# Kernel tuning notes

Hardware: AMD Instinct MI355X
Metric: run time of the kernel (lower is better)

Reference implementation:

```python
import jax, jax.numpy as jnp
import numpy as np

B, N, DIM = 8, 1024, 1024
H, DH = 16, 64           # heads, dim_head; inner_dim = H*DH = 1024
SCALE = DH ** -0.5


def setup_inputs() -> dict:
    key = jax.random.key(0)
    k_x, k_qkv, k_out, k_b = jax.random.split(key, 4)
    inner = H * DH
    x = jax.random.normal(k_x, (B, N, DIM), dtype=jnp.float32)
    # nn.Linear(dim, inner*3, bias=False): y = x @ W_qkv
    W_qkv = jax.random.normal(k_qkv, (DIM, 3 * inner), dtype=jnp.float32) * (DIM ** -0.5)
    # nn.Linear(inner, dim) with bias (project_out is True since heads!=1)
    W_out = jax.random.normal(k_out, (inner, DIM), dtype=jnp.float32) * (inner ** -0.5)
    b_out = jax.random.normal(k_b, (DIM,), dtype=jnp.float32) * 0.01
    return {"x": x, "W_qkv": W_qkv, "W_out": W_out, "b_out": b_out}


def reference(x, W_qkv, W_out, b_out):
    # 'trans' branch of Attention.forward (dropout p=0 -> identity)
    qkv = x @ W_qkv                                   # [b, n, 3*inner]
    q, k, v = jnp.split(qkv, 3, axis=-1)              # each [b, n, inner]
    def to_heads(t):
        b, n, _ = t.shape
        return t.reshape(b, n, H, DH).transpose(0, 2, 1, 3)  # [b, h, n, d]
    q, k, v = to_heads(q), to_heads(k), to_heads(v)
    dots = jnp.einsum('bhid,bhjd->bhij', q, k) * SCALE  # [b, h, n, n]
    attn = jax.nn.softmax(dots, axis=-1)
    out = jnp.einsum('bhij,bhjd->bhid', attn, v)        # [b, h, n, d]
    # original sets attn = out (b h n d) before merging heads
    attn_ret = out
    out_m = out.transpose(0, 2, 1, 3).reshape(B, N, H * DH)  # [b, n, inner]
    proj = out_m @ W_out + b_out                        # [b, n, dim]
    return (proj, attn_ret)
```

## Files before the change

### kernel.cpp

```cpp
#include <hip/hip_runtime.h>
#include <hip/hip_bf16.h>
#include <math.h>

typedef __bf16 bf16_t;
typedef __bf16 bf16x8 __attribute__((ext_vector_type(8)));
typedef __bf16 bf16x4 __attribute__((ext_vector_type(4)));
typedef float f32x4 __attribute__((ext_vector_type(4)));

#define MFMA16(a, b, c) __builtin_amdgcn_mfma_f32_16x16x32_bf16((a), (b), (c), 0, 0, 0)

#define AS3(p) ((__attribute__((address_space(3))) void*)(p))
#define AS1(p) ((const __attribute__((address_space(1))) void*)(p))

#define B_ 8
#define N_ 1024
#define DIM_ 1024
#define H_ 16
#define DH_ 64

#define QSCALE 0.18033688011112042f
#define SM_SHIFT 12.0f

__global__ __launch_bounds__(256) void k_convert(const float* __restrict__ in,
                                                 bf16_t* __restrict__ out) {
    size_t idx = ((size_t)blockIdx.x * 256 + threadIdx.x) * 8;
    f32x4 a = *(const f32x4*)(in + idx);
    f32x4 b = *(const f32x4*)(in + idx + 4);
    bf16x8 o;
    o[0] = (bf16_t)a[0]; o[1] = (bf16_t)a[1]; o[2] = (bf16_t)a[2]; o[3] = (bf16_t)a[3];
    o[4] = (bf16_t)b[0]; o[5] = (bf16_t)b[1]; o[6] = (bf16_t)b[2]; o[7] = (bf16_t)b[3];
    *(bf16x8*)(out + idx) = o;
}

__global__ __launch_bounds__(256) void k_prep_w(const float* __restrict__ Wqkv,
                                                bf16_t* __restrict__ wqkvt,
                                                const float* __restrict__ Wout,
                                                bf16_t* __restrict__ woutt) {
    __shared__ float tile[32][33];
    int bx = blockIdx.x;
    const float* in;
    bf16_t* out;
    int C, cb;
    if (bx < 96) { in = Wqkv; out = wqkvt; C = 3072; cb = bx; }
    else         { in = Wout; out = woutt; C = 1024; cb = bx - 96; }
    const int R = 1024;
    int c0 = cb * 32, r0 = blockIdx.y * 32;
    int tx = threadIdx.x, ty = threadIdx.y;
#pragma unroll
    for (int i = 0; i < 4; ++i)
        tile[ty + 8 * i][tx] = in[(size_t)(r0 + ty + 8 * i) * C + (c0 + tx)];
    __syncthreads();
#pragma unroll
    for (int i = 0; i < 4; ++i)
        out[(size_t)(c0 + ty + 8 * i) * R + (r0 + tx)] = (bf16_t)tile[tx][ty + 8 * i];
}

__global__ __launch_bounds__(256, 2) void k_gemm_qkv(const bf16_t* __restrict__ A,
                                                     const bf16_t* __restrict__ Bt,
                                                     bf16_t* __restrict__ qb,
                                                     bf16_t* __restrict__ kbuf,
                                                     bf16_t* __restrict__ vtb) {
    __shared__ __align__(16) bf16_t As[256 * 64];
    __shared__ __align__(16) bf16_t Bs[128 * 64];
    int tid = threadIdx.x;
    int lane = tid & 63, wave = tid >> 6;
    int quad = lane >> 4, l16 = lane & 15;
    int m0 = blockIdx.y * 256, c0 = blockIdx.x * 128;
    int wm = (wave & 1) * 128, wn = (wave >> 1) * 64;

    const f32x4 vzero = {0.f, 0.f, 0.f, 0.f};
    f32x4 acc[8][4];
#pragma unroll
    for (int i = 0; i < 8; ++i)
#pragma unroll
        for (int j = 0; j < 4; ++j) acc[i][j] = vzero;

    for (int k0 = 0; k0 < 1024; k0 += 64) {
#pragma unroll
        for (int i = 0; i < 8; ++i) {
            int cid = tid + 256 * i;
            int row = cid >> 3;
            int g = (cid & 7) ^ (row & 7);
            __builtin_amdgcn_global_load_lds(
                AS1(A + (size_t)(m0 + row) * 1024 + k0 + g * 8), AS3(As + cid * 8), 16, 0, 0);
        }
#pragma unroll
        for (int i = 0; i < 4; ++i) {
            int cid = tid + 256 * i;
            int row = cid >> 3;
            int g = (cid & 7) ^ (row & 7);
            __builtin_amdgcn_global_load_lds(
                AS1(Bt + (size_t)(c0 + row) * 1024 + k0 + g * 8), AS3(Bs + cid * 8), 16, 0, 0);
        }
        __syncthreads();
#pragma unroll
        for (int c = 0; c < 2; ++c) {
            int s = (4 * c + quad) ^ (l16 & 7);
            bf16x8 bfr[4];
#pragma unroll
            for (int j = 0; j < 4; ++j)
                bfr[j] = *(const bf16x8*)(Bs + (wn + 16 * j + l16) * 64 + s * 8);
#pragma unroll
            for (int i = 0; i < 8; ++i) {
                bf16x8 af = *(const bf16x8*)(As + (wm + 16 * i + l16) * 64 + s * 8);
#pragma unroll
                for (int j = 0; j < 4; ++j)
                    acc[i][j] = MFMA16(af, bfr[j], acc[i][j]);
            }
        }
        __syncthreads();
    }

    int tsel = c0 >> 10;
#pragma unroll
    for (int i = 0; i < 8; ++i) {
#pragma unroll
        for (int r = 0; r < 4; ++r) {
            int m = m0 + wm + 16 * i + quad * 4 + r;
            int b = m >> 10, n = m & 1023;
#pragma unroll
            for (int j = 0; j < 4; ++j) {
                int cc = c0 + wn + 16 * j + l16;
                int ic = cc & 1023;
                int h = ic >> 6, d = ic & 63;
                float val = acc[i][j][r];
                if (tsel == 0)
                    qb[(((size_t)b * H_ + h) * N_ + n) * DH_ + d] = (bf16_t)(val * QSCALE);
                else if (tsel == 1)
                    kbuf[(((size_t)b * H_ + h) * N_ + n) * DH_ + d] = (bf16_t)val;
                else
                    vtb[(((size_t)b * H_ + h) * DH_ + d) * N_ + n] = (bf16_t)val;
            }
        }
    }
}

__global__ __launch_bounds__(256, 2) void k_attn(const bf16_t* __restrict__ q,
                                                 const bf16_t* __restrict__ k,
                                                 const bf16_t* __restrict__ vt,
                                                 float* __restrict__ oattn,
                                                 bf16_t* __restrict__ outm) {
    __shared__ __align__(16) bf16_t Ks[64 * 64];
    __shared__ __align__(16) bf16_t Vs[64 * 64];
    __shared__ __align__(16) bf16_t Ps[4 * 4 * 16 * 72];
    int tid = threadIdx.x;
    int lane = tid & 63, wave = tid >> 6;
    int quad = lane >> 4, l16 = lane & 15;
    int qt = blockIdx.x & 3;
    int bh = blockIdx.x >> 2;
    int b = bh >> 4, h = bh & 15;

    const bf16_t* qp = q + ((size_t)bh * N_ + qt * 256 + wave * 64) * DH_;
    bf16x8 qa[4][2];
#pragma unroll
    for (int g = 0; g < 4; ++g)
#pragma unroll
        for (int c = 0; c < 2; ++c)
            qa[g][c] = *(const bf16x8*)(qp + (size_t)(g * 16 + l16) * DH_ + c * 32 + quad * 8);

    const bf16_t* kp = k + (size_t)bh * N_ * DH_;
    const bf16_t* vp = vt + (size_t)bh * DH_ * N_;
    bf16_t* Pw = Ps + wave * (4 * 16 * 72);

    const f32x4 vzero = {0.f, 0.f, 0.f, 0.f};
    f32x4 o[4][4];
#pragma unroll
    for (int g = 0; g < 4; ++g)
#pragma unroll
        for (int t = 0; t < 4; ++t) o[g][t] = vzero;
    float lsum[4] = {0.f, 0.f, 0.f, 0.f};

    for (int kb = 0; kb < 16; ++kb) {
#pragma unroll
        for (int i = 0; i < 2; ++i) {
            int cid = tid + 256 * i;
            int row = cid >> 3;
            int g = (cid & 7) ^ (row & 7);
            __builtin_amdgcn_global_load_lds(
                AS1(kp + (size_t)(kb * 64 + row) * DH_ + g * 8), AS3(Ks + cid * 8), 16, 0, 0);
            __builtin_amdgcn_global_load_lds(
                AS1(vp + (size_t)row * N_ + kb * 64 + g * 8), AS3(Vs + cid * 8), 16, 0, 0);
        }
        __syncthreads();

        f32x4 st[4][4];
#pragma unroll
        for (int jt = 0; jt < 4; ++jt) {
#pragma unroll
            for (int g = 0; g < 4; ++g) st[g][jt] = vzero;
#pragma unroll
            for (int c = 0; c < 2; ++c) {
                int s = (4 * c + quad) ^ (l16 & 7);
                bf16x8 kf = *(const bf16x8*)(Ks + (16 * jt + l16) * 64 + s * 8);
#pragma unroll
                for (int g = 0; g < 4; ++g)
                    st[g][jt] = MFMA16(kf, qa[g][c], st[g][jt]);
            }
        }

#pragma unroll
        for (int g = 0; g < 4; ++g) {
            float ps = 0.f;
#pragma unroll
            for (int jt = 0; jt < 4; ++jt) {
                bf16x4 pk;
#pragma unroll
                for (int r = 0; r < 4; ++r) {
                    float p = __builtin_amdgcn_exp2f(st[g][jt][r] - SM_SHIFT);
                    ps += p;
                    pk[r] = (bf16_t)p;
                }
                *(bf16x4*)(Pw + g * (16 * 72) + l16 * 72 + jt * 16 + quad * 4) = pk;
            }
            lsum[g] += ps;
        }

        bf16x8 pf[4][2];
#pragma unroll
        for (int g = 0; g < 4; ++g)
#pragma unroll
            for (int c = 0; c < 2; ++c)
                pf[g][c] = *(const bf16x8*)(Pw + g * (16 * 72) + l16 * 72 + c * 32 + quad * 8);
#pragma unroll
        for (int t = 0; t < 4; ++t)
#pragma unroll
            for (int c = 0; c < 2; ++c) {
                int s = (4 * c + quad) ^ (l16 & 7);
                bf16x8 vf = *(const bf16x8*)(Vs + (16 * t + l16) * 64 + s * 8);
#pragma unroll
                for (int g = 0; g < 4; ++g)
                    o[g][t] = MFMA16(vf, pf[g][c], o[g][t]);
            }
        __syncthreads();
    }

#pragma unroll
    for (int g = 0; g < 4; ++g) {
        lsum[g] += __shfl_xor(lsum[g], 16);
        lsum[g] += __shfl_xor(lsum[g], 32);
    }

    float* Ot = (float*)Ps + wave * 16 * 68;
#pragma unroll
    for (int g = 0; g < 4; ++g) {
        float inv = 1.f / lsum[g];
#pragma unroll
        for (int t = 0; t < 4; ++t) {
            f32x4 v4;
#pragma unroll
            for (int r = 0; r < 4; ++r) v4[r] = o[g][t][r] * inv;
            *(f32x4*)(Ot + l16 * 68 + t * 16 + quad * 4) = v4;
        }
        int row = lane >> 2, cl = lane & 3;
        int n = qt * 256 + wave * 64 + g * 16 + row;
        const float* orow = Ot + row * 68 + cl * 16;
        float* gout = oattn + ((size_t)bh * N_ + n) * DH_ + cl * 16;
        bf16_t* gm = outm + ((size_t)b * N_ + n) * DIM_ + h * DH_ + cl * 16;
#pragma unroll
        for (int s = 0; s < 4; ++s) {
            f32x4 v = *(const f32x4*)(orow + s * 4);
            *(f32x4*)(gout + s * 4) = v;
            bf16x4 vb;
#pragma unroll
            for (int r = 0; r < 4; ++r) vb[r] = (bf16_t)v[r];
            *(bf16x4*)(gm + s * 4) = vb;
        }
    }
}

__global__ __launch_bounds__(256) void k_gemm_proj(const bf16_t* __restrict__ A,
                                                   const bf16_t* __restrict__ Bt,
                                                   const float* __restrict__ bias,
                                                   float* __restrict__ out) {
    __shared__ __align__(16) bf16_t As[128 * 64];
    __shared__ __align__(16) bf16_t Bs[128 * 64];
    int tid = threadIdx.x;
    int lane = tid & 63, wave = tid >> 6;
    int quad = lane >> 4, l16 = lane & 15;
    int m0 = blockIdx.y * 128, c0 = blockIdx.x * 128;
    int wm = (wave & 1) * 64, wn = (wave >> 1) * 64;

    const f32x4 vzero = {0.f, 0.f, 0.f, 0.f};
    f32x4 acc[4][4];
#pragma unroll
    for (int i = 0; i < 4; ++i)
#pragma unroll
        for (int j = 0; j < 4; ++j) acc[i][j] = vzero;

    for (int k0 = 0; k0 < 1024; k0 += 64) {
#pragma unroll
        for (int i = 0; i < 4; ++i) {
            int cid = tid + 256 * i;
            int row = cid >> 3;
            int g = (cid & 7) ^ (row & 7);
            __builtin_amdgcn_global_load_lds(
                AS1(A + (size_t)(m0 + row) * 1024 + k0 + g * 8), AS3(As + cid * 8), 16, 0, 0);
            __builtin_amdgcn_global_load_lds(
                AS1(Bt + (size_t)(c0 + row) * 1024 + k0 + g * 8), AS3(Bs + cid * 8), 16, 0, 0);
        }
        __syncthreads();
#pragma unroll
        for (int c = 0; c < 2; ++c) {
            int s = (4 * c + quad) ^ (l16 & 7);
            bf16x8 bfr[4];
#pragma unroll
            for (int j = 0; j < 4; ++j)
                bfr[j] = *(const bf16x8*)(Bs + (wn + 16 * j + l16) * 64 + s * 8);
#pragma unroll
            for (int i = 0; i < 4; ++i) {
                bf16x8 af = *(const bf16x8*)(As + (wm + 16 * i + l16) * 64 + s * 8);
#pragma unroll
                for (int j = 0; j < 4; ++j)
                    acc[i][j] = MFMA16(af, bfr[j], acc[i][j]);
            }
        }
        __syncthreads();
    }

#pragma unroll
    for (int i = 0; i < 4; ++i) {
#pragma unroll
        for (int r = 0; r < 4; ++r) {
            int m = m0 + wm + 16 * i + quad * 4 + r;
#pragma unroll
            for (int j = 0; j < 4; ++j) {
                int cc = c0 + wn + 16 * j + l16;
                out[(size_t)m * DIM_ + cc] = acc[i][j][r] + bias[cc];
            }
        }
    }
}

extern "C" void kernel_launch(void* const* d_in, const int* in_sizes, int n_in,
                              void* d_out, int out_size, void* d_ws, size_t ws_size,
                              hipStream_t stream) {
    const float* x    = (const float*)d_in[0];
    const float* Wqkv = (const float*)d_in[1];
    const float* Wout = (const float*)d_in[2];
    const float* bout = (const float*)d_in[3];

    float* proj  = (float*)d_out;
    float* oattn = proj + (size_t)B_ * N_ * DIM_;

    char* ws = (char*)d_ws;
    const size_t MB = 1024 * 1024;
    bf16_t* xb    = (bf16_t*)(ws);
    bf16_t* wqkvt = (bf16_t*)(ws + 16 * MB);
    bf16_t* woutt = (bf16_t*)(ws + 22 * MB);
    bf16_t* qb    = (bf16_t*)(ws + 24 * MB);
    bf16_t* kbuf  = (bf16_t*)(ws + 40 * MB);
    bf16_t* vtb   = (bf16_t*)(ws + 56 * MB);
    bf16_t* outm  = (bf16_t*)(ws + 72 * MB);

    k_convert<<<4096, 256, 0, stream>>>(x, xb);
    k_prep_w<<<dim3(128, 32), dim3(32, 8), 0, stream>>>(Wqkv, wqkvt, Wout, woutt);
    k_gemm_qkv<<<dim3(24, 32), 256, 0, stream>>>(xb, wqkvt, qb, kbuf, vtb);
    k_attn<<<512, 256, 0, stream>>>(qb, kbuf, vtb, oattn, outm);
    k_gemm_proj<<<dim3(8, 64), 256, 0, stream>>>(outm, woutt, bout, proj);
}
```

Measured before the change: 281.2 us.

## Restructure QKV GEMM with 256x256 tiles, double-buffered LDS and block swizzle

The QKV projection GEMM moves from 256x128 tiles with 4 waves to 256x256 tiles with 8 waves. LDS is double-buffered so global-to-LDS loads for step t+2 are issued while step t computes, using vmcnt waits and raw barriers. The launch becomes a 1D grid with a swizzled block-to-tile mapping intended to improve L2 reuse, and MFMA bursts are wrapped in setprio. LDS use per block doubles (128KB), which limits blocks per CU, and the grid drops to 384 blocks, which may not fill all CUs evenly.

```diff
diff --git a/kernel.cpp b/kernel.cpp
--- a/kernel.cpp
+++ b/kernel.cpp
@@ -55,18 +55,22 @@
         out[(size_t)(c0 + ty + 8 * i) * R + (r0 + tx)] = (bf16_t)tile[tx][ty + 8 * i];
 }
 
-__global__ __launch_bounds__(256, 2) void k_gemm_qkv(const bf16_t* __restrict__ A,
+__global__ __launch_bounds__(512, 2) void k_gemm_qkv(const bf16_t* __restrict__ A,
                                                      const bf16_t* __restrict__ Bt,
                                                      bf16_t* __restrict__ qb,
                                                      bf16_t* __restrict__ kbuf,
                                                      bf16_t* __restrict__ vtb) {
-    __shared__ __align__(16) bf16_t As[256 * 64];
-    __shared__ __align__(16) bf16_t Bs[128 * 64];
+    __shared__ __align__(16) bf16_t As[2][256 * 64];
+    __shared__ __align__(16) bf16_t Bs[2][256 * 64];
     int tid = threadIdx.x;
     int lane = tid & 63, wave = tid >> 6;
     int quad = lane >> 4, l16 = lane & 15;
-    int m0 = blockIdx.y * 256, c0 = blockIdx.x * 128;
-    int wm = (wave & 1) * 128, wn = (wave >> 1) * 64;
+    int wr = wave >> 2, wc = wave & 3;
+
+    int bid = blockIdx.x;
+    int swz = (bid & 7) * 48 + (bid >> 3);
+    int mt = swz / 12, nt = swz % 12;
+    int m0 = mt * 256, c0 = nt * 256;
 
     const f32x4 vzero = {0.f, 0.f, 0.f, 0.f};
     f32x4 acc[8][4];
@@ -75,52 +79,124 @@
 #pragma unroll
         for (int j = 0; j < 4; ++j) acc[i][j] = vzero;
 
-    for (int k0 = 0; k0 < 1024; k0 += 64) {
-#pragma unroll
-        for (int i = 0; i < 8; ++i) {
-            int cid = tid + 256 * i;
+    int s0 = ((quad) ^ (l16 & 7)) * 8;
+    int s1 = ((4 + quad) ^ (l16 & 7)) * 8;
+
+    auto stage = [&](int t) {
+        int k0 = t * 64;
+        bf16_t* Ad = &As[t & 1][0];
+        bf16_t* Bd = &Bs[t & 1][0];
+#pragma unroll
+        for (int i = 0; i < 4; ++i) {
+            int cid = tid + 512 * i;
             int row = cid >> 3;
             int g = (cid & 7) ^ (row & 7);
             __builtin_amdgcn_global_load_lds(
-                AS1(A + (size_t)(m0 + row) * 1024 + k0 + g * 8), AS3(As + cid * 8), 16, 0, 0);
+                AS1(A + (size_t)(m0 + row) * 1024 + k0 + g * 8), AS3(Ad + cid * 8), 16, 0, 0);
         }
 #pragma unroll
         for (int i = 0; i < 4; ++i) {
-            int cid = tid + 256 * i;
+            int cid = tid + 512 * i;
             int row = cid >> 3;
             int g = (cid & 7) ^ (row & 7);
             __builtin_amdgcn_global_load_lds(
-                AS1(Bt + (size_t)(c0 + row) * 1024 + k0 + g * 8), AS3(Bs + cid * 8), 16, 0, 0);
-        }
-        __syncthreads();
-#pragma unroll
-        for (int c = 0; c < 2; ++c) {
-            int s = (4 * c + quad) ^ (l16 & 7);
-            bf16x8 bfr[4];
-#pragma unroll
-            for (int j = 0; j < 4; ++j)
-                bfr[j] = *(const bf16x8*)(Bs + (wn + 16 * j + l16) * 64 + s * 8);
-#pragma unroll
-            for (int i = 0; i < 8; ++i) {
-                bf16x8 af = *(const bf16x8*)(As + (wm + 16 * i + l16) * 64 + s * 8);
-#pragma unroll
-                for (int j = 0; j < 4; ++j)
-                    acc[i][j] = MFMA16(af, bfr[j], acc[i][j]);
-            }
-        }
-        __syncthreads();
-    }
-
-    int tsel = c0 >> 10;
+                AS1(Bt + (size_t)(c0 + row) * 1024 + k0 + g * 8), AS3(Bd + cid * 8), 16, 0, 0);
+        }
+    };
+
+    stage(0);
+    stage(1);
+
+#pragma unroll 2
+    for (int t = 0; t < 16; ++t) {
+        int cur = t & 1;
+        if (t < 15)
+            asm volatile("s_waitcnt vmcnt(8)" ::: "memory");
+        else
+            asm volatile("s_waitcnt vmcnt(0)" ::: "memory");
+        __builtin_amdgcn_s_barrier();
+        asm volatile("" ::: "memory");
+
+        const bf16_t* Arow = &As[cur][0] + (size_t)(wr * 128 + l16) * 64;
+        const bf16_t* Brow = &Bs[cur][0] + (size_t)(wc * 64 + l16) * 64;
+
+        bf16x8 af[4][2], bq0[2][2], bq1[2][2];
+
+#pragma unroll
+        for (int i = 0; i < 4; ++i) {
+            af[i][0] = *(const bf16x8*)(Arow + (16 * i) * 64 + s0);
+            af[i][1] = *(const bf16x8*)(Arow + (16 * i) * 64 + s1);
+        }
+#pragma unroll
+        for (int j = 0; j < 2; ++j) {
+            bq0[j][0] = *(const bf16x8*)(Brow + (16 * j) * 64 + s0);
+            bq0[j][1] = *(const bf16x8*)(Brow + (16 * j) * 64 + s1);
+        }
+        __builtin_amdgcn_s_setprio(1);
+#pragma unroll
+        for (int i = 0; i < 4; ++i)
+#pragma unroll
+            for (int j = 0; j < 2; ++j) {
+                acc[i][j] = MFMA16(af[i][0], bq0[j][0], acc[i][j]);
+                acc[i][j] = MFMA16(af[i][1], bq0[j][1], acc[i][j]);
+            }
+        __builtin_amdgcn_s_setprio(0);
+
+#pragma unroll
+        for (int j = 0; j < 2; ++j) {
+            bq1[j][0] = *(const bf16x8*)(Brow + (32 + 16 * j) * 64 + s0);
+            bq1[j][1] = *(const bf16x8*)(Brow + (32 + 16 * j) * 64 + s1);
+        }
+        __builtin_amdgcn_s_setprio(1);
+#pragma unroll
+        for (int i = 0; i < 4; ++i)
+#pragma unroll
+            for (int j = 0; j < 2; ++j) {
+                acc[i][2 + j] = MFMA16(af[i][0], bq1[j][0], acc[i][2 + j]);
+                acc[i][2 + j] = MFMA16(af[i][1], bq1[j][1], acc[i][2 + j]);
+            }
+        __builtin_amdgcn_s_setprio(0);
+
+#pragma unroll
+        for (int i = 0; i < 4; ++i) {
+            af[i][0] = *(const bf16x8*)(Arow + (64 + 16 * i) * 64 + s0);
+            af[i][1] = *(const bf16x8*)(Arow + (64 + 16 * i) * 64 + s1);
+        }
+        __builtin_amdgcn_s_setprio(1);
+#pragma unroll
+        for (int i = 0; i < 4; ++i)
+#pragma unroll
+            for (int j = 0; j < 2; ++j) {
+                acc[4 + i][2 + j] = MFMA16(af[i][0], bq1[j][0], acc[4 + i][2 + j]);
+                acc[4 + i][2 + j] = MFMA16(af[i][1], bq1[j][1], acc[4 + i][2 + j]);
+            }
+        __builtin_amdgcn_s_setprio(0);
+
+        __builtin_amdgcn_s_setprio(1);
+#pragma unroll
+        for (int i = 0; i < 4; ++i)
+#pragma unroll
+            for (int j = 0; j < 2; ++j) {
+                acc[4 + i][j] = MFMA16(af[i][0], bq0[j][0], acc[4 + i][j]);
+                acc[4 + i][j] = MFMA16(af[i][1], bq0[j][1], acc[4 + i][j]);
+            }
+        __builtin_amdgcn_s_setprio(0);
+
+        asm volatile("" ::: "memory");
+        __builtin_amdgcn_s_barrier();
+        if (t + 2 < 16) stage(t + 2);
+    }
+
+    int tsel = nt >> 2;
 #pragma unroll
     for (int i = 0; i < 8; ++i) {
 #pragma unroll
         for (int r = 0; r < 4; ++r) {
-            int m = m0 + wm + 16 * i + quad * 4 + r;
+            int m = m0 + wr * 128 + 16 * i + quad * 4 + r;
             int b = m >> 10, n = m & 1023;
 #pragma unroll
             for (int j = 0; j < 4; ++j) {
-                int cc = c0 + wn + 16 * j + l16;
+                int cc = c0 + wc * 64 + 16 * j + l16;
                 int ic = cc & 1023;
                 int h = ic >> 6, d = ic & 63;
                 float val = acc[i][j][r];
@@ -354,7 +430,7 @@
 
     k_convert<<<4096, 256, 0, stream>>>(x, xb);
     k_prep_w<<<dim3(128, 32), dim3(32, 8), 0, stream>>>(Wqkv, wqkvt, Wout, woutt);
-    k_gemm_qkv<<<dim3(24, 32), 256, 0, stream>>>(xb, wqkvt, qb, kbuf, vtb);
+    k_gemm_qkv<<<384, 512, 0, stream>>>(xb, wqkvt, qb, kbuf, vtb);
     k_attn<<<512, 256, 0, stream>>>(qb, kbuf, vtb, oattn, outm);
     k_gemm_proj<<<dim3(8, 64), 256, 0, stream>>>(outm, woutt, bout, proj);
 }
```

Result: no change. 278.0 us (-1.2%).

## Merge prep kernels, write V row-major then transpose in a separate kernel

Applied to the files above, without the earlier changes.

Merges the x conversion and the weight transposes into one launch. The QKV GEMM epilogue now writes V in the same head-major row layout as Q and K, using a single branch-free store path. A new LDS-tiled kernel then transposes V into the layout the attention kernel expects. The goal is to remove the scattered, uncoalesced transposed V stores from the GEMM epilogue, at the cost of an extra launch and an extra read and write of V. The GEMM occupancy hint is also raised from 2 to 3 blocks per SIMD.

```diff
diff --git a/kernel.cpp b/kernel.cpp
--- a/kernel.cpp
+++ b/kernel.cpp
@@ -21,31 +21,35 @@
 #define QSCALE 0.18033688011112042f
 #define SM_SHIFT 12.0f
 
-__global__ __launch_bounds__(256) void k_convert(const float* __restrict__ in,
-                                                 bf16_t* __restrict__ out) {
-    size_t idx = ((size_t)blockIdx.x * 256 + threadIdx.x) * 8;
-    f32x4 a = *(const f32x4*)(in + idx);
-    f32x4 b = *(const f32x4*)(in + idx + 4);
-    bf16x8 o;
-    o[0] = (bf16_t)a[0]; o[1] = (bf16_t)a[1]; o[2] = (bf16_t)a[2]; o[3] = (bf16_t)a[3];
-    o[4] = (bf16_t)b[0]; o[5] = (bf16_t)b[1]; o[6] = (bf16_t)b[2]; o[7] = (bf16_t)b[3];
-    *(bf16x8*)(out + idx) = o;
-}
-
-__global__ __launch_bounds__(256) void k_prep_w(const float* __restrict__ Wqkv,
-                                                bf16_t* __restrict__ wqkvt,
-                                                const float* __restrict__ Wout,
-                                                bf16_t* __restrict__ woutt) {
+__global__ __launch_bounds__(256) void k_prep(const float* __restrict__ x,
+                                              bf16_t* __restrict__ xb,
+                                              const float* __restrict__ Wqkv,
+                                              bf16_t* __restrict__ wqkvt,
+                                              const float* __restrict__ Wout,
+                                              bf16_t* __restrict__ woutt) {
+    int bx = blockIdx.x;
+    int tid = threadIdx.x;
+    if (bx < 4096) {
+        size_t idx = ((size_t)bx * 256 + tid) * 8;
+        f32x4 a = *(const f32x4*)(x + idx);
+        f32x4 b = *(const f32x4*)(x + idx + 4);
+        bf16x8 o;
+        o[0] = (bf16_t)a[0]; o[1] = (bf16_t)a[1]; o[2] = (bf16_t)a[2]; o[3] = (bf16_t)a[3];
+        o[4] = (bf16_t)b[0]; o[5] = (bf16_t)b[1]; o[6] = (bf16_t)b[2]; o[7] = (bf16_t)b[3];
+        *(bf16x8*)(xb + idx) = o;
+        return;
+    }
     __shared__ float tile[32][33];
-    int bx = blockIdx.x;
+    int idx = bx - 4096;
+    int rb = idx >> 7, cbx = idx & 127;
     const float* in;
     bf16_t* out;
     int C, cb;
-    if (bx < 96) { in = Wqkv; out = wqkvt; C = 3072; cb = bx; }
-    else         { in = Wout; out = woutt; C = 1024; cb = bx - 96; }
+    if (cbx < 96) { in = Wqkv; out = wqkvt; C = 3072; cb = cbx; }
+    else          { in = Wout; out = woutt; C = 1024; cb = cbx - 96; }
     const int R = 1024;
-    int c0 = cb * 32, r0 = blockIdx.y * 32;
-    int tx = threadIdx.x, ty = threadIdx.y;
+    int c0 = cb * 32, r0 = rb * 32;
+    int tx = tid & 31, ty = tid >> 5;
 #pragma unroll
     for (int i = 0; i < 4; ++i)
         tile[ty + 8 * i][tx] = in[(size_t)(r0 + ty + 8 * i) * C + (c0 + tx)];
@@ -55,11 +59,11 @@
         out[(size_t)(c0 + ty + 8 * i) * R + (r0 + tx)] = (bf16_t)tile[tx][ty + 8 * i];
 }
 
-__global__ __launch_bounds__(256, 2) void k_gemm_qkv(const bf16_t* __restrict__ A,
+__global__ __launch_bounds__(256, 3) void k_gemm_qkv(const bf16_t* __restrict__ A,
                                                      const bf16_t* __restrict__ Bt,
                                                      bf16_t* __restrict__ qb,
                                                      bf16_t* __restrict__ kbuf,
-                                                     bf16_t* __restrict__ vtb) {
+                                                     bf16_t* __restrict__ vbuf) {
     __shared__ __align__(16) bf16_t As[256 * 64];
     __shared__ __align__(16) bf16_t Bs[128 * 64];
     int tid = threadIdx.x;
@@ -112,6 +116,8 @@
     }
 
     int tsel = c0 >> 10;
+    bf16_t* obase = (tsel == 0) ? qb : (tsel == 1) ? kbuf : vbuf;
+    float scl = (tsel == 0) ? QSCALE : 1.0f;
 #pragma unroll
     for (int i = 0; i < 8; ++i) {
 #pragma unroll
@@ -123,16 +129,31 @@
                 int cc = c0 + wn + 16 * j + l16;
                 int ic = cc & 1023;
                 int h = ic >> 6, d = ic & 63;
-                float val = acc[i][j][r];
-                if (tsel == 0)
-                    qb[(((size_t)b * H_ + h) * N_ + n) * DH_ + d] = (bf16_t)(val * QSCALE);
-                else if (tsel == 1)
-                    kbuf[(((size_t)b * H_ + h) * N_ + n) * DH_ + d] = (bf16_t)val;
-                else
-                    vtb[(((size_t)b * H_ + h) * DH_ + d) * N_ + n] = (bf16_t)val;
-            }
-        }
-    }
+                obase[(((size_t)b * H_ + h) * N_ + n) * DH_ + d] = (bf16_t)(acc[i][j][r] * scl);
+            }
+        }
+    }
+}
+
+__global__ __launch_bounds__(256) void k_prep_v(const bf16_t* __restrict__ in,
+                                                bf16_t* __restrict__ out) {
+    __shared__ bf16_t t[64][65];
+    int bh = blockIdx.y;
+    int n0 = blockIdx.x * 64;
+    int tid = threadIdx.x;
+    int r = tid >> 2, c = (tid & 3) * 16;
+    const bf16_t* ip = in + ((size_t)bh * N_ + n0 + r) * DH_ + c;
+    bf16x8 a = *(const bf16x8*)ip;
+    bf16x8 b2 = *(const bf16x8*)(ip + 8);
+#pragma unroll
+    for (int e = 0; e < 8; ++e) { t[r][c + e] = a[e]; t[r][c + 8 + e] = b2[e]; }
+    __syncthreads();
+    bf16x8 o1, o2;
+#pragma unroll
+    for (int e = 0; e < 8; ++e) { o1[e] = t[c + e][r]; o2[e] = t[c + 8 + e][r]; }
+    bf16_t* op = out + ((size_t)bh * DH_ + r) * N_ + n0 + c;
+    *(bf16x8*)op = o1;
+    *(bf16x8*)(op + 8) = o2;
 }
 
 __global__ __launch_bounds__(256, 2) void k_attn(const bf16_t* __restrict__ q,
@@ -351,10 +372,11 @@
     bf16_t* kbuf  = (bf16_t*)(ws + 40 * MB);
     bf16_t* vtb   = (bf16_t*)(ws + 56 * MB);
     bf16_t* outm  = (bf16_t*)(ws + 72 * MB);
-
-    k_convert<<<4096, 256, 0, stream>>>(x, xb);
-    k_prep_w<<<dim3(128, 32), dim3(32, 8), 0, stream>>>(Wqkv, wqkvt, Wout, woutt);
-    k_gemm_qkv<<<dim3(24, 32), 256, 0, stream>>>(xb, wqkvt, qb, kbuf, vtb);
+    bf16_t* vbuf  = outm;
+
+    k_prep<<<8192, 256, 0, stream>>>(x, xb, Wqkv, wqkvt, Wout, woutt);
+    k_gemm_qkv<<<dim3(24, 32), 256, 0, stream>>>(xb, wqkvt, qb, kbuf, vbuf);
+    k_prep_v<<<dim3(16, 128), 256, 0, stream>>>(vbuf, vtb);
     k_attn<<<512, 256, 0, stream>>>(qb, kbuf, vtb, oattn, outm);
     k_gemm_proj<<<dim3(8, 64), 256, 0, stream>>>(outm, woutt, bout, proj);
 }
```

Result: faster. 275.6 us (-2.0%).
